# Kernel tuning notes

Hardware: AMD Instinct MI355X
Metric: run time of the kernel (lower is better)

## Reference

```python
import jax, jax.numpy as jnp
import numpy as np
from jax.scipy.linalg import expm

DIM = 128
BF = 2          # branching_factor
H = 8           # num_heads
MAX_DEPTH = 12
PAD = BF + 1    # padding value used by pad_sequence in the torch module
N = 256         # number of positions


def setup_inputs() -> dict:
    key = jax.random.key(0)
    k1, k2 = jax.random.split(key)
    # raw _primitives parameter (the torch init applies softmax+cumsum to rand;
    # any values work for the math -- only the skew-hermitian part matters)
    prim = jax.random.uniform(k1, (BF * H + 1, DIM, DIM), dtype=jnp.float32)
    positions = jax.random.randint(k2, (N,), 0, BF ** MAX_DEPTH)  # node indices, >= 0
    return {"primitives_param": prim, "positions": positions}


def _path_words(positions):
    """Vectorized equivalent of create_paths + pad_sequence.

    For node index n the branch path is built by walking up the tree:
    branch = (n-1) % BF, parent = (n-1) // BF. Digits come out leaf->root,
    so we reverse the valid prefix and right-pad with PAD to MAX_DEPTH.
    """
    d = positions.astype(jnp.int32)
    digs = []
    for _ in range(MAX_DEPTH):
        valid = d > 0
        digs.append(jnp.where(valid, (d - 1) % BF, PAD))
        d = jnp.where(valid, (d - 1) // BF, 0)
    R = jnp.stack(digs, axis=1)            # (N, 12) leaf->root digits
    depth = jnp.sum(R != PAD, axis=1)       # path length per token
    idx = depth[:, None] - 1 - jnp.arange(MAX_DEPTH)[None, :]
    pw = jnp.take_along_axis(R, jnp.clip(idx, 0, MAX_DEPTH - 1), axis=1)
    pw = jnp.where(idx >= 0, pw, PAD)       # (N, 12) root->leaf, PAD-padded
    return pw, depth


def reference(primitives_param, positions):
    pw, depth = _path_words(positions)

    # ---- steps matrix (tree distance), mirrors the no_grad block ----
    pm = pw != PAD                                        # (N, 12)
    mask = pm[:, None, :] & pm[None, :, :]                # (N, N, 12)
    eq = pw[:, None, :] == pw[None, :, :]
    common = jnp.cumprod(eq.astype(jnp.int32), axis=-1).astype(bool) & mask
    cpl = common.sum(-1)                                  # common prefix length
    steps = depth[:, None] + depth[None, :] - 2 * cpl     # (N, N) int

    # ---- unitary primitives: expm of the skew(-hermitian, real) part ----
    skew = primitives_param - jnp.swapaxes(primitives_param, -1, -2)
    prims = expm(skew)                                    # (BF*H+1, DIM, DIM)
    sos = prims[-1]
    P = prims[:-1].reshape(BF, H, DIM, DIM)

    n_tok = pw.shape[0]
    maps = jnp.broadcast_to(jnp.eye(DIM, dtype=prims.dtype)[None, None],
                            (n_tok, H, DIM, DIM))
    sos_ptr = pw[:, 0] == -1                              # never true for pos>=0, kept for fidelity
    maps = jnp.where(sos_ptr[:, None, None, None], sos[None, None], maps)

    # fused gather-indexed scan over tree depth: instead of BF masked matmuls
    # per depth, gather each token's branch primitive and do one batched matmul.
    for d in range(MAX_DEPTH):
        sel = pw[:, d]                                    # (N,) in {0..BF-1} or PAD
        Pk = P[jnp.clip(sel, 0, BF - 1)]                  # (N, H, DIM, DIM)
        new = jnp.einsum('nhij,nhjk->nhik', maps, Pk)
        maps = jnp.where((sel < BF)[:, None, None, None], new, maps)

    return maps, steps
```

## Files before the change

### kernel.cpp

```cpp
#include <hip/hip_runtime.h>

typedef unsigned short ushort_t;
typedef unsigned int uint_t;
typedef __attribute__((ext_vector_type(8))) short bf16x8;
typedef __attribute__((ext_vector_type(4))) float f32x4;

#define NMAT 16
#define MSZ 16384

__device__ __forceinline__ ushort_t f32_bf16(float f) {
  uint_t u = __builtin_bit_cast(uint_t, f);
  u += 0x7FFFu + ((u >> 16) & 1u);
  return (ushort_t)(u >> 16);
}

__device__ __forceinline__ float bf16_f32(ushort_t b) {
  uint_t u = ((uint_t)b) << 16;
  return __builtin_bit_cast(float, u);
}

__device__ __forceinline__ int swz(int r, int k) {
  return r * 128 + (((k >> 3) ^ (r & 7)) << 3) + (k & 7);
}

__device__ __forceinline__ void mm_frag(const ushort_t* U, const ushort_t* V,
                                        int r0, int c0, int quad, int l16,
                                        f32x4 (&acc)[4][4]) {
#pragma unroll
  for (int rt = 0; rt < 4; rt++)
#pragma unroll
    for (int ct = 0; ct < 4; ct++) {
      f32x4 z = {0.f, 0.f, 0.f, 0.f};
      acc[rt][ct] = z;
    }
#pragma unroll
  for (int kt = 0; kt < 4; kt++) {
    int k = kt * 32 + quad * 8;
    bf16x8 a[4], b[4];
#pragma unroll
    for (int rt = 0; rt < 4; rt++) a[rt] = *(const bf16x8*)(&U[swz(r0 + rt * 16 + l16, k)]);
#pragma unroll
    for (int ct = 0; ct < 4; ct++) b[ct] = *(const bf16x8*)(&V[swz(c0 + ct * 16 + l16, k)]);
#pragma unroll
    for (int rt = 0; rt < 4; rt++)
#pragma unroll
      for (int ct = 0; ct < 4; ct++)
        acc[rt][ct] = __builtin_amdgcn_mfma_f32_16x16x32_bf16(a[rt], b[ct], acc[rt][ct], 0, 0, 0);
  }
}

__device__ __forceinline__ void store_T(ushort_t* dst, const f32x4 (&acc)[4][4],
                                        int r0, int c0, int quad, int l16,
                                        float scale, float cdiag) {
#pragma unroll
  for (int rt = 0; rt < 4; rt++)
#pragma unroll
    for (int ct = 0; ct < 4; ct++) {
      int dr = r0 + rt * 16 + quad * 4, dc = c0 + ct * 16 + l16;
      float v[4];
#pragma unroll
      for (int i = 0; i < 4; i++) {
        v[i] = scale * acc[rt][ct][i];
        if (dr + i == dc) v[i] += cdiag;
      }
      uint2 pk;
      pk.x = (uint_t)f32_bf16(v[0]) | ((uint_t)f32_bf16(v[1]) << 16);
      pk.y = (uint_t)f32_bf16(v[2]) | ((uint_t)f32_bf16(v[3]) << 16);
      *(uint2*)(&dst[swz(dc, dr)]) = pk;
    }
}

__device__ __forceinline__ void set_ident(ushort_t* dst, int t, float c) {
  ushort_t cb = f32_bf16(c);
  for (int i = 0; i < 64; i++) {
    int e = i * 256 + t;
    int r = e >> 7, k = e & 127;
    dst[swz(r, k)] = (r == k) ? cb : (ushort_t)0;
  }
}

__global__ __launch_bounds__(256, 1) void expm1_kernel(const float* __restrict__ prim,
                                                       ushort_t* __restrict__ wsCS) {
  __shared__ ushort_t __align__(16) bufA[MSZ];
  __shared__ ushort_t __align__(16) bufB[MSZ];
  int kmat = blockIdx.x >> 1, which = blockIdx.x & 1;
  int t = threadIdx.x, wave = t >> 6, lane = t & 63;
  int quad = lane >> 4, l16 = lane & 15;
  int r0 = (wave >> 1) * 64, c0 = (wave & 1) * 64;
  const float* p = prim + kmat * MSZ;

  for (int i = 0; i < 64; i++) {
    int e = i * 256 + t;
    int r = e >> 7, c = e & 127;
    bufA[swz(r, c)] = f32_bf16((p[r * 128 + c] - p[c * 128 + r]) * 0.125f);
  }
  __syncthreads();

  f32x4 acc[4][4];
  mm_frag(bufA, bufA, r0, c0, quad, l16, acc);
  __syncthreads();
  store_T(bufB, acc, r0, c0, quad, l16, -1.f, 0.f);
  __syncthreads();

  float coef[9];
  if (which == 0) {
    coef[0] = 1.f; coef[1] = 1.f / 2; coef[2] = 1.f / 24; coef[3] = 1.f / 720;
    coef[4] = 1.f / 40320; coef[5] = 1.f / 3628800.f; coef[6] = 1.f / 479001600.f;
    coef[7] = 1.f / 87178291200.f; coef[8] = 1.f / 20922789888000.f;
  } else {
    coef[0] = 1.f; coef[1] = 1.f / 6; coef[2] = 1.f / 120; coef[3] = 1.f / 5040;
    coef[4] = 1.f / 362880.f; coef[5] = 1.f / 39916800.f; coef[6] = 1.f / 6227020800.f;
    coef[7] = 1.f / 1307674368000.f; coef[8] = 1.f / 355687428096000.f;
  }
  set_ident(bufA, t, coef[8]);
  __syncthreads();
#pragma unroll
  for (int k = 7; k >= 0; k--) {
    mm_frag(bufB, bufA, r0, c0, quad, l16, acc);
    __syncthreads();
    store_T(bufA, acc, r0, c0, quad, l16, 1.f, coef[k]);
    __syncthreads();
  }
  ushort_t* dst = wsCS + (size_t)(which * NMAT + kmat) * MSZ;
  for (int i = 0; i < 8; i++) {
    int e = (i * 256 + t) * 8;
    int r = e >> 7, k = e & 127;
    *(uint4*)(dst + e) = *(const uint4*)(&bufA[swz(r, k)]);
  }
}

__global__ __launch_bounds__(256, 1) void expm2_kernel(
    const float* __restrict__ prim, const ushort_t* __restrict__ wsCS,
    ushort_t* __restrict__ PN, ushort_t* __restrict__ PT) {
  __shared__ ushort_t __align__(16) bufA[MSZ];
  __shared__ ushort_t __align__(16) bufB[MSZ];
  int kmat = blockIdx.x;
  int t = threadIdx.x, wave = t >> 6, lane = t & 63;
  int quad = lane >> 4, l16 = lane & 15;
  int r0 = (wave >> 1) * 64, c0 = (wave & 1) * 64;
  const float* p = prim + kmat * MSZ;
  const ushort_t* Cg = wsCS + (size_t)kmat * MSZ;
  const ushort_t* Sg = wsCS + (size_t)(NMAT + kmat) * MSZ;

  for (int i = 0; i < 64; i++) {
    int e = i * 256 + t;
    int r = e >> 7, c = e & 127;
    bufA[swz(r, c)] = f32_bf16((p[r * 128 + c] - p[c * 128 + r]) * 0.125f);
  }
  for (int i = 0; i < 8; i++) {
    int e = (i * 256 + t) * 8;
    int r = e >> 7, k = e & 127;
    *(uint4*)(&bufB[swz(r, k)]) = *(const uint4*)(Sg + e);
  }
  __syncthreads();

  f32x4 acc[4][4];
  mm_frag(bufA, bufB, r0, c0, quad, l16, acc);
  __syncthreads();
#pragma unroll
  for (int rt = 0; rt < 4; rt++)
#pragma unroll
    for (int ct = 0; ct < 4; ct++) {
      int dr = r0 + rt * 16 + quad * 4, dc = c0 + ct * 16 + l16;
      uint2 cp = *(const uint2*)(Cg + dc * 128 + dr);
      float cf[4] = {bf16_f32((ushort_t)(cp.x & 0xffff)), bf16_f32((ushort_t)(cp.x >> 16)),
                     bf16_f32((ushort_t)(cp.y & 0xffff)), bf16_f32((ushort_t)(cp.y >> 16))};
      uint2 en, et;
      en.x = (uint_t)f32_bf16(cf[0] - acc[rt][ct][0]) | ((uint_t)f32_bf16(cf[1] - acc[rt][ct][1]) << 16);
      en.y = (uint_t)f32_bf16(cf[2] - acc[rt][ct][2]) | ((uint_t)f32_bf16(cf[3] - acc[rt][ct][3]) << 16);
      et.x = (uint_t)f32_bf16(cf[0] + acc[rt][ct][0]) | ((uint_t)f32_bf16(cf[1] + acc[rt][ct][1]) << 16);
      et.y = (uint_t)f32_bf16(cf[2] + acc[rt][ct][2]) | ((uint_t)f32_bf16(cf[3] + acc[rt][ct][3]) << 16);
      *(uint2*)(&bufA[swz(dc, dr)]) = en;
      *(uint2*)(&bufB[swz(dc, dr)]) = et;
    }
  __syncthreads();

#pragma unroll 1
  for (int sq = 0; sq < 3; sq++) {
    mm_frag(bufA, bufB, r0, c0, quad, l16, acc);
    __syncthreads();
#pragma unroll
    for (int rt = 0; rt < 4; rt++)
#pragma unroll
      for (int ct = 0; ct < 4; ct++) {
        int dr = r0 + rt * 16 + quad * 4, dc = c0 + ct * 16 + l16;
        uint2 pk;
        pk.x = (uint_t)f32_bf16(acc[rt][ct][0]) | ((uint_t)f32_bf16(acc[rt][ct][1]) << 16);
        pk.y = (uint_t)f32_bf16(acc[rt][ct][2]) | ((uint_t)f32_bf16(acc[rt][ct][3]) << 16);
        *(uint2*)(&bufB[swz(dc, dr)]) = pk;
#pragma unroll
        for (int i = 0; i < 4; i++) bufA[swz(dr + i, dc)] = f32_bf16(acc[rt][ct][i]);
      }
    __syncthreads();
  }
  for (int i = 0; i < 8; i++) {
    int e = (i * 256 + t) * 8;
    int r = e >> 7, k = e & 127;
    *(uint4*)(PN + (size_t)kmat * MSZ + e) = *(const uint4*)(&bufA[swz(r, k)]);
    *(uint4*)(PT + (size_t)kmat * MSZ + e) = *(const uint4*)(&bufB[swz(r, k)]);
  }
}

__global__ void steps_kernel(const int* __restrict__ pos, float* __restrict__ os, int N) {
  int i = blockIdx.x, j = threadIdx.x;
  int mi = pos[i] + 1, mj = pos[j] + 1;
  int di = 31 - __builtin_clz((unsigned)mi);
  int dj = 31 - __builtin_clz((unsigned)mj);
  int tt = di < dj ? di : dj;
  unsigned x = (unsigned)((mi >> (di - tt)) ^ (mj >> (dj - tt)));
  int cpl = tt - (x ? (32 - __builtin_clz(x)) : 0);
  os[i * N + j] = (float)(di + dj - 2 * cpl);
}

#define STEP_BODY(A)                                                                    \
  _Pragma("unroll") for (int kt = 0; kt < 4; kt++) {                                    \
    int k = kt * 32 + quad * 8;                                                         \
    bf16x8 b[4];                                                                        \
    _Pragma("unroll") for (int ct = 0; ct < 4; ct++)                                    \
        b[ct] = *(const bf16x8*)(&Lr[swz(c0 + ct * 16 + l16, k)]);                      \
    _Pragma("unroll") for (int rt = 0; rt < 4; rt++)                                    \
        _Pragma("unroll") for (int ct = 0; ct < 4; ct++)                                \
            acc[rt][ct] = __builtin_amdgcn_mfma_f32_16x16x32_bf16(A[kt][rt], b[ct],     \
                                                                  acc[rt][ct], 0, 0, 0); \
  }

__global__ __launch_bounds__(256, 2) void maps_kernel(
    const ushort_t* __restrict__ PN, const ushort_t* __restrict__ PT,
    const int* __restrict__ positions, float* __restrict__ out) {
  __shared__ ushort_t __align__(16) Mb[2][MSZ];
  int bx = blockIdx.x;
  int n = bx >> 3, h = bx & 7;
  int t = threadIdx.x, wave = t >> 6, lane = t & 63;
  int quad = lane >> 4, l16 = lane & 15;
  int m = positions[n] + 1;
  int depth = 31 - __builtin_clz((unsigned)m);
  float* ob = out + (size_t)(n * 8 + h) * MSZ;

  if (depth == 0) {
    for (int i = 0; i < 64; i++) {
      int e = i * 256 + t;
      int r = e >> 7, k = e & 127;
      ob[e] = (r == k) ? 1.0f : 0.0f;
    }
    return;
  }
  int d0 = (m >> (depth - 1)) & 1;
  if (depth == 1) {
    const ushort_t* src = PN + (size_t)(d0 * 8 + h) * MSZ;
    for (int i = 0; i < 64; i++) {
      int e = i * 256 + t;
      ob[e] = bf16_f32(src[e]);
    }
    return;
  }

  int r0 = (wave >> 1) * 64, c0 = (wave & 1) * 64;
  const ushort_t* pt0 = PT + (size_t)h * MSZ;
  const ushort_t* pt1 = PT + (size_t)(8 + h) * MSZ;
  bf16x8 a0[4][4], a1[4][4];
#pragma unroll
  for (int kt = 0; kt < 4; kt++)
#pragma unroll
    for (int rt = 0; rt < 4; rt++) {
      int off = (r0 + rt * 16 + l16) * 128 + kt * 32 + quad * 8;
      a0[kt][rt] = *(const bf16x8*)(pt0 + off);
      a1[kt][rt] = *(const bf16x8*)(pt1 + off);
    }
  {
    const ushort_t* src = PN + (size_t)(d0 * 8 + h) * MSZ;
#pragma unroll
    for (int i = 0; i < 8; i++) {
      int e = (i * 256 + t) * 8;
      int r = e >> 7, k = e & 127;
      *(uint4*)(&Mb[0][swz(r, k)]) = *(const uint4*)(src + e);
    }
  }
  __syncthreads();

  int cur = 0;
  for (int s = 1; s < depth; s++) {
    int sel = (m >> (depth - 1 - s)) & 1;
    const ushort_t* Lr = Mb[cur];
    ushort_t* Lw = Mb[cur ^ 1];
    f32x4 acc[4][4];
#pragma unroll
    for (int rt = 0; rt < 4; rt++)
#pragma unroll
      for (int ct = 0; ct < 4; ct++) {
        f32x4 z = {0.f, 0.f, 0.f, 0.f};
        acc[rt][ct] = z;
      }
    if (sel) { STEP_BODY(a1) } else { STEP_BODY(a0) }

    if (s == depth - 1) {
#pragma unroll
      for (int rt = 0; rt < 4; rt++)
#pragma unroll
        for (int ct = 0; ct < 4; ct++) {
          int dr = r0 + rt * 16 + quad * 4;
          int dc = c0 + ct * 16 + l16;
          *(f32x4*)(ob + dc * 128 + dr) = acc[rt][ct];
        }
    } else {
#pragma unroll
      for (int rt = 0; rt < 4; rt++)
#pragma unroll
        for (int ct = 0; ct < 4; ct++) {
          int dr = r0 + rt * 16 + quad * 4;
          int dc = c0 + ct * 16 + l16;
          uint2 pk;
          pk.x = (uint_t)f32_bf16(acc[rt][ct][0]) | ((uint_t)f32_bf16(acc[rt][ct][1]) << 16);
          pk.y = (uint_t)f32_bf16(acc[rt][ct][2]) | ((uint_t)f32_bf16(acc[rt][ct][3]) << 16);
          *(uint2*)(&Lw[swz(dc, dr)]) = pk;
        }
      __syncthreads();
      cur ^= 1;
    }
  }
}

extern "C" void kernel_launch(void* const* d_in, const int* in_sizes, int n_in,
                              void* d_out, int out_size, void* d_ws, size_t ws_size,
                              hipStream_t stream) {
  const float* prim = (const float*)d_in[0];
  const int* positions = (const int*)d_in[1];
  int N = in_sizes[1];
  float* out = (float*)d_out;

  ushort_t* wsCS = (ushort_t*)d_ws;
  ushort_t* PN = wsCS + 2 * NMAT * MSZ;
  ushort_t* PT = PN + NMAT * MSZ;

  steps_kernel<<<N, N, 0, stream>>>(positions, out + (size_t)N * 8 * MSZ, N);
  expm1_kernel<<<2 * NMAT, 256, 0, stream>>>(prim, wsCS);
  expm2_kernel<<<NMAT, 256, 0, stream>>>(prim, wsCS, PN, PT);
  maps_kernel<<<N * 8, 256, 0, stream>>>(PN, PT, positions, out);
}
```

Measured before the change: 252.0 us.

## Precompute 4-level product tables and evaluate Taylor polynomial in Y=X^2

Precomputes products of primitive matrices for all branch words of length 2, 3 and 4 in new table kernels. The per-token scan then does one matmul per 4 tree levels instead of one per level, cutting the number of serial 128x128 matmuls per token by about four. The expm Taylor polynomial is also rewritten to be evaluated in Y=X^2 with a Horner scheme that folds the odd terms in elementwise, halving its serial matmuls. The cost is two extra small launches, a larger workspace table, and an extra bf16 rounding at each precomputed product.

```diff
diff --git a/kernel.cpp b/kernel.cpp
--- a/kernel.cpp
+++ b/kernel.cpp
@@ -21,6 +21,10 @@
 
 __device__ __forceinline__ int swz(int r, int k) {
   return r * 128 + (((k >> 3) ^ (r & 7)) << 3) + (k & 7);
+}
+
+__device__ __forceinline__ int tab_off(int L) {
+  return (L == 1) ? 0 : (L == 2) ? 2 : (L == 3) ? 6 : 14;
 }
 
 __device__ __forceinline__ void mm_frag(const ushort_t* U, const ushort_t* V,
@@ -102,6 +106,19 @@
   store_T(bufB, acc, r0, c0, quad, l16, -1.f, 0.f);
   __syncthreads();
 
+  uint2 yv[4][4];
+#pragma unroll
+  for (int rt = 0; rt < 4; rt++)
+#pragma unroll
+    for (int ct = 0; ct < 4; ct++) {
+      int dr = r0 + rt * 16 + quad * 4, dc = c0 + ct * 16 + l16;
+      yv[rt][ct] = *(const uint2*)(&bufB[swz(dc, dr)]);
+    }
+
+  mm_frag(bufB, bufB, r0, c0, quad, l16, acc);
+  __syncthreads();
+  store_T(bufB, acc, r0, c0, quad, l16, 1.f, 0.f);
+
   float coef[9];
   if (which == 0) {
     coef[0] = 1.f; coef[1] = 1.f / 2; coef[2] = 1.f / 24; coef[3] = 1.f / 720;
@@ -112,13 +129,34 @@
     coef[4] = 1.f / 362880.f; coef[5] = 1.f / 39916800.f; coef[6] = 1.f / 6227020800.f;
     coef[7] = 1.f / 1307674368000.f; coef[8] = 1.f / 355687428096000.f;
   }
+
   set_ident(bufA, t, coef[8]);
   __syncthreads();
-#pragma unroll
-  for (int k = 7; k >= 0; k--) {
+
+#pragma unroll
+  for (int k = 3; k >= 0; k--) {
     mm_frag(bufB, bufA, r0, c0, quad, l16, acc);
     __syncthreads();
-    store_T(bufA, acc, r0, c0, quad, l16, 1.f, coef[k]);
+    float cd = coef[2 * k], cy = coef[2 * k + 1];
+#pragma unroll
+    for (int rt = 0; rt < 4; rt++)
+#pragma unroll
+      for (int ct = 0; ct < 4; ct++) {
+        int dr = r0 + rt * 16 + quad * 4, dc = c0 + ct * 16 + l16;
+        uint2 yp = yv[rt][ct];
+        float y[4] = {bf16_f32((ushort_t)(yp.x & 0xffff)), bf16_f32((ushort_t)(yp.x >> 16)),
+                      bf16_f32((ushort_t)(yp.y & 0xffff)), bf16_f32((ushort_t)(yp.y >> 16))};
+        float v[4];
+#pragma unroll
+        for (int i = 0; i < 4; i++) {
+          v[i] = acc[rt][ct][i] + cy * y[i];
+          if (dr + i == dc) v[i] += cd;
+        }
+        uint2 pk;
+        pk.x = (uint_t)f32_bf16(v[0]) | ((uint_t)f32_bf16(v[1]) << 16);
+        pk.y = (uint_t)f32_bf16(v[2]) | ((uint_t)f32_bf16(v[3]) << 16);
+        *(uint2*)(&bufA[swz(dc, dr)]) = pk;
+      }
     __syncthreads();
   }
   ushort_t* dst = wsCS + (size_t)(which * NMAT + kmat) * MSZ;
@@ -201,6 +239,67 @@
   }
 }
 
+__global__ __launch_bounds__(256) void table_kernel(ushort_t* __restrict__ TN,
+                                                    ushort_t* __restrict__ TT, int mode) {
+  int bx = blockIdx.x;
+  int eA, eB, eO, h;
+  if (mode == 0) {
+    int c = bx >> 3; h = bx & 7;
+    eA = c >> 1; eB = c & 1; eO = 2 + c;
+  } else if (bx < 64) {
+    int c = bx >> 3; h = bx & 7;
+    eA = 2 + (c >> 1); eB = c & 1; eO = 6 + c;
+  } else {
+    int c = (bx - 64) >> 3; h = (bx - 64) & 7;
+    eA = 2 + (c >> 2); eB = 2 + (c & 3); eO = 14 + c;
+  }
+  int t = threadIdx.x, wave = t >> 6, lane = t & 63;
+  int quad = lane >> 4, l16 = lane & 15;
+  int r0 = (wave >> 1) * 64, c0 = (wave & 1) * 64;
+  const ushort_t* A = TN + ((size_t)eA * 8 + h) * MSZ;
+  const ushort_t* B = TT + ((size_t)eB * 8 + h) * MSZ;
+  ushort_t* oN = TN + ((size_t)eO * 8 + h) * MSZ;
+  ushort_t* oT = TT + ((size_t)eO * 8 + h) * MSZ;
+
+  bf16x8 a[4][4], b[4][4];
+#pragma unroll
+  for (int kt = 0; kt < 4; kt++) {
+#pragma unroll
+    for (int rt = 0; rt < 4; rt++)
+      a[kt][rt] = *(const bf16x8*)(A + (r0 + rt * 16 + l16) * 128 + kt * 32 + quad * 8);
+#pragma unroll
+    for (int ct = 0; ct < 4; ct++)
+      b[kt][ct] = *(const bf16x8*)(B + (c0 + ct * 16 + l16) * 128 + kt * 32 + quad * 8);
+  }
+  f32x4 acc[4][4];
+#pragma unroll
+  for (int rt = 0; rt < 4; rt++)
+#pragma unroll
+    for (int ct = 0; ct < 4; ct++) {
+      f32x4 z = {0.f, 0.f, 0.f, 0.f};
+      acc[rt][ct] = z;
+    }
+#pragma unroll
+  for (int kt = 0; kt < 4; kt++)
+#pragma unroll
+    for (int rt = 0; rt < 4; rt++)
+#pragma unroll
+      for (int ct = 0; ct < 4; ct++)
+        acc[rt][ct] = __builtin_amdgcn_mfma_f32_16x16x32_bf16(a[kt][rt], b[kt][ct], acc[rt][ct], 0, 0, 0);
+#pragma unroll
+  for (int rt = 0; rt < 4; rt++)
+#pragma unroll
+    for (int ct = 0; ct < 4; ct++) {
+      int dr = r0 + rt * 16 + quad * 4, dc = c0 + ct * 16 + l16;
+      uint2 pk;
+      pk.x = (uint_t)f32_bf16(acc[rt][ct][0]) | ((uint_t)f32_bf16(acc[rt][ct][1]) << 16);
+      pk.y = (uint_t)f32_bf16(acc[rt][ct][2]) | ((uint_t)f32_bf16(acc[rt][ct][3]) << 16);
+      *(uint2*)(oT + dc * 128 + dr) = pk;
+#pragma unroll
+      for (int i = 0; i < 4; i++) oN[(dr + i) * 128 + dc] = f32_bf16(acc[rt][ct][i]);
+    }
+}
+
 __global__ void steps_kernel(const int* __restrict__ pos, float* __restrict__ os, int N) {
   int i = blockIdx.x, j = threadIdx.x;
   int mi = pos[i] + 1, mj = pos[j] + 1;
@@ -212,20 +311,8 @@
   os[i * N + j] = (float)(di + dj - 2 * cpl);
 }
 
-#define STEP_BODY(A)                                                                    \
-  _Pragma("unroll") for (int kt = 0; kt < 4; kt++) {                                    \
-    int k = kt * 32 + quad * 8;                                                         \
-    bf16x8 b[4];                                                                        \
-    _Pragma("unroll") for (int ct = 0; ct < 4; ct++)                                    \
-        b[ct] = *(const bf16x8*)(&Lr[swz(c0 + ct * 16 + l16, k)]);                      \
-    _Pragma("unroll") for (int rt = 0; rt < 4; rt++)                                    \
-        _Pragma("unroll") for (int ct = 0; ct < 4; ct++)                                \
-            acc[rt][ct] = __builtin_amdgcn_mfma_f32_16x16x32_bf16(A[kt][rt], b[ct],     \
-                                                                  acc[rt][ct], 0, 0, 0); \
-  }
-
 __global__ __launch_bounds__(256, 2) void maps_kernel(
-    const ushort_t* __restrict__ PN, const ushort_t* __restrict__ PT,
+    const ushort_t* __restrict__ TN, const ushort_t* __restrict__ TT,
     const int* __restrict__ positions, float* __restrict__ out) {
   __shared__ ushort_t __align__(16) Mb[2][MSZ];
   int bx = blockIdx.x;
@@ -244,44 +331,42 @@
     }
     return;
   }
-  int d0 = (m >> (depth - 1)) & 1;
-  if (depth == 1) {
-    const ushort_t* src = PN + (size_t)(d0 * 8 + h) * MSZ;
-    for (int i = 0; i < 64; i++) {
-      int e = i * 256 + t;
-      ob[e] = bf16_f32(src[e]);
-    }
-    return;
-  }
-
-  int r0 = (wave >> 1) * 64, c0 = (wave & 1) * 64;
-  const ushort_t* pt0 = PT + (size_t)h * MSZ;
-  const ushort_t* pt1 = PT + (size_t)(8 + h) * MSZ;
-  bf16x8 a0[4][4], a1[4][4];
-#pragma unroll
-  for (int kt = 0; kt < 4; kt++)
-#pragma unroll
-    for (int rt = 0; rt < 4; rt++) {
-      int off = (r0 + rt * 16 + l16) * 128 + kt * 32 + quad * 8;
-      a0[kt][rt] = *(const bf16x8*)(pt0 + off);
-      a1[kt][rt] = *(const bf16x8*)(pt1 + off);
-    }
-  {
-    const ushort_t* src = PN + (size_t)(d0 * 8 + h) * MSZ;
-#pragma unroll
+
+  int K = (depth + 3) >> 2;
+  int L0 = depth - 4 * (K - 1);
+  int c0v = (m >> (depth - L0)) & ((1 << L0) - 1);
+  const ushort_t* src0 = TN + ((size_t)(tab_off(L0) + c0v) * 8 + h) * MSZ;
+
+  if (K == 1) {
     for (int i = 0; i < 8; i++) {
       int e = (i * 256 + t) * 8;
-      int r = e >> 7, k = e & 127;
-      *(uint4*)(&Mb[0][swz(r, k)]) = *(const uint4*)(src + e);
-    }
-  }
-  __syncthreads();
-
+      bf16x8 v = *(const bf16x8*)(src0 + e);
+#pragma unroll
+      for (int j = 0; j < 8; j++) ob[e + j] = bf16_f32((ushort_t)v[j]);
+    }
+    return;
+  }
+
+  int r0 = (wave >> 1) * 64, c0 = (wave & 1) * 64;
+#pragma unroll
+  for (int i = 0; i < 8; i++) {
+    int e = (i * 256 + t) * 8;
+    int r = e >> 7, k = e & 127;
+    *(uint4*)(&Mb[0][swz(r, k)]) = *(const uint4*)(src0 + e);
+  }
+  __syncthreads();
+
+  int rem = depth - L0;
   int cur = 0;
-  for (int s = 1; s < depth; s++) {
-    int sel = (m >> (depth - 1 - s)) & 1;
-    const ushort_t* Lr = Mb[cur];
-    ushort_t* Lw = Mb[cur ^ 1];
+  while (rem > 0) {
+    int cb = (m >> (rem - 4)) & 15;
+    const ushort_t* Ap = TT + ((size_t)(14 + cb) * 8 + h) * MSZ;
+    bf16x8 a[4][4];
+#pragma unroll
+    for (int kt = 0; kt < 4; kt++)
+#pragma unroll
+      for (int rt = 0; rt < 4; rt++)
+        a[kt][rt] = *(const bf16x8*)(Ap + (r0 + rt * 16 + l16) * 128 + kt * 32 + quad * 8);
     f32x4 acc[4][4];
 #pragma unroll
     for (int rt = 0; rt < 4; rt++)
@@ -290,9 +375,21 @@
         f32x4 z = {0.f, 0.f, 0.f, 0.f};
         acc[rt][ct] = z;
       }
-    if (sel) { STEP_BODY(a1) } else { STEP_BODY(a0) }
-
-    if (s == depth - 1) {
+    const ushort_t* Lr = Mb[cur];
+#pragma unroll
+    for (int kt = 0; kt < 4; kt++) {
+      int k = kt * 32 + quad * 8;
+      bf16x8 b[4];
+#pragma unroll
+      for (int ct = 0; ct < 4; ct++) b[ct] = *(const bf16x8*)(&Lr[swz(c0 + ct * 16 + l16, k)]);
+#pragma unroll
+      for (int rt = 0; rt < 4; rt++)
+#pragma unroll
+        for (int ct = 0; ct < 4; ct++)
+          acc[rt][ct] = __builtin_amdgcn_mfma_f32_16x16x32_bf16(a[kt][rt], b[ct], acc[rt][ct], 0, 0, 0);
+    }
+    rem -= 4;
+    if (rem == 0) {
 #pragma unroll
       for (int rt = 0; rt < 4; rt++)
 #pragma unroll
@@ -302,6 +399,7 @@
           *(f32x4*)(ob + dc * 128 + dr) = acc[rt][ct];
         }
     } else {
+      ushort_t* Lw = Mb[cur ^ 1];
 #pragma unroll
       for (int rt = 0; rt < 4; rt++)
 #pragma unroll
@@ -328,11 +426,13 @@
   float* out = (float*)d_out;
 
   ushort_t* wsCS = (ushort_t*)d_ws;
-  ushort_t* PN = wsCS + 2 * NMAT * MSZ;
-  ushort_t* PT = PN + NMAT * MSZ;
+  ushort_t* TN = wsCS + (size_t)2 * NMAT * MSZ;
+  ushort_t* TT = TN + (size_t)240 * MSZ;
 
   steps_kernel<<<N, N, 0, stream>>>(positions, out + (size_t)N * 8 * MSZ, N);
   expm1_kernel<<<2 * NMAT, 256, 0, stream>>>(prim, wsCS);
-  expm2_kernel<<<NMAT, 256, 0, stream>>>(prim, wsCS, PN, PT);
-  maps_kernel<<<N * 8, 256, 0, stream>>>(PN, PT, positions, out);
-}
+  expm2_kernel<<<NMAT, 256, 0, stream>>>(prim, wsCS, TN, TT);
+  table_kernel<<<32, 256, 0, stream>>>(TN, TT, 0);
+  table_kernel<<<192, 256, 0, stream>>>(TN, TT, 1);
+  maps_kernel<<<(size_t)N * 8, 256, 0, stream>>>(TN, TT, positions, out);
+}
```

After: 224.3 us. -11.0%, faster.
